# Kernel tuning notes

Hardware: AMD Instinct MI355X
Metric: run time of the kernel (lower is better)

The kernel has to match this reference:

```python
import jax, jax.numpy as jnp
import numpy as np

NUM_HEADS = 4
NUM_GROUPS = 32
EPS = 1e-5

def setup_inputs() -> dict:
    key = jax.random.key(0)
    ks = jax.random.split(key, 3)
    B, C, H, W = 16, 512, 32, 32
    x = jax.random.normal(ks[0], (B, C, H, W), dtype=jnp.float32)
    gn_w = jnp.ones((C,), jnp.float32)
    gn_b = jnp.zeros((C,), jnp.float32)
    qkv_w = jax.random.normal(ks[1], (3 * C, C), dtype=jnp.float32) * (C ** -0.5)
    qkv_b = jnp.zeros((3 * C,), jnp.float32)
    proj_w = jax.random.normal(ks[2], (C, C), dtype=jnp.float32) * (C ** -0.5)
    proj_b = jnp.zeros((C,), jnp.float32)
    return {"x": x, "gn_w": gn_w, "gn_b": gn_b, "qkv_w": qkv_w,
            "qkv_b": qkv_b, "proj_w": proj_w, "proj_b": proj_b}

def group_norm(x, w, b):
    B, C, H, W = x.shape
    xg = x.reshape(B, NUM_GROUPS, C // NUM_GROUPS, H, W)
    mean = xg.mean(axis=(2, 3, 4), keepdims=True)
    var = xg.var(axis=(2, 3, 4), keepdims=True)
    xg = (xg - mean) * jax.lax.rsqrt(var + EPS)
    x = xg.reshape(B, C, H, W)
    return x * w[None, :, None, None] + b[None, :, None, None]

def reference(x, gn_w, gn_b, qkv_w, qkv_b, proj_w, proj_b):
    B, C, H, W = x.shape
    hd = C // NUM_HEADS
    h = group_norm(x, gn_w, gn_b)
    # 1x1 conv == channel matmul
    qkv = jnp.einsum('oc,bchw->bohw', qkv_w, h) + qkv_b[None, :, None, None]
    q, k, v = jnp.split(qkv, 3, axis=1)
    N = H * W
    q = q.reshape(B, NUM_HEADS, hd, N)
    k = k.reshape(B, NUM_HEADS, hd, N)
    v = v.reshape(B, NUM_HEADS, hd, N)
    scale = hd ** -0.5
    attn = jnp.einsum('bhcn,bhcm->bhnm', q, k) * scale
    attn = jax.nn.softmax(attn, axis=-1)
    o = jnp.einsum('bhnm,bhcm->bhcn', attn, v).reshape(B, C, H, W)
    o = jnp.einsum('oc,bchw->bohw', proj_w, o) + proj_b[None, :, None, None]
    return x + o
```

## Files before the change

### kernel.cpp

```cpp
#include <hip/hip_runtime.h>

typedef __attribute__((ext_vector_type(4))) float f32x4;
typedef __attribute__((ext_vector_type(8))) short s16x8;

#define MFMA16(a, b, c) __builtin_amdgcn_mfma_f32_16x16x32_bf16((a), (b), (c), 0, 0, 0)

__device__ __forceinline__ unsigned short f2bf(float f) {
    union { float f; unsigned u; } v; v.f = f;
    unsigned u = v.u + 0x7FFFu + ((v.u >> 16) & 1u);
    return (unsigned short)(u >> 16);
}

__device__ __forceinline__ unsigned cvtpk(float lo, float hi) {
    unsigned r;
    asm("v_cvt_pk_bf16_f32 %0, %1, %2" : "=v"(r) : "v"(lo), "v"(hi));
    return r;
}

__device__ __forceinline__ float exp2f_fast(float x) {
    float r;
    asm("v_exp_f32 %0, %1" : "=v"(r) : "v"(x));
    return r;
}

__device__ __forceinline__ void gll16(const unsigned short* g, unsigned short* l) {
    __builtin_amdgcn_global_load_lds((const __attribute__((address_space(1))) void*)g,
                                     (__attribute__((address_space(3))) void*)l, 16, 0, 0);
}

__global__ __launch_bounds__(256) void k_wconv(const float* __restrict__ qkv_w,
                                               const float* __restrict__ proj_w,
                                               unsigned short* __restrict__ wout) {
    int i = blockIdx.x * 256 + threadIdx.x;
    const int NQ = 3 * 512 * 512;
    float v = (i < NQ) ? qkv_w[i] : proj_w[i - NQ];
    wout[i] = f2bf(v);
}

__global__ __launch_bounds__(256) void k_gnstats(const float* __restrict__ x,
                                                 float* __restrict__ stats) {
    int bg = blockIdx.x;
    const float4* p = (const float4*)(x + (size_t)bg * 16384);
    float s = 0.f, ss = 0.f;
    for (int i = threadIdx.x; i < 4096; i += 256) {
        float4 v = p[i];
        s += v.x + v.y + v.z + v.w;
        ss += v.x * v.x + v.y * v.y + v.z * v.z + v.w * v.w;
    }
    for (int w = 1; w < 64; w <<= 1) { s += __shfl_xor(s, w); ss += __shfl_xor(ss, w); }
    __shared__ float rs[4], rss[4];
    int wid = threadIdx.x >> 6;
    if ((threadIdx.x & 63) == 0) { rs[wid] = s; rss[wid] = ss; }
    __syncthreads();
    if (threadIdx.x == 0) {
        float S = rs[0] + rs[1] + rs[2] + rs[3];
        float SS = rss[0] + rss[1] + rss[2] + rss[3];
        float mean = S * (1.f / 16384.f);
        float var = SS * (1.f / 16384.f) - mean * mean;
        stats[bg * 2] = mean;
        stats[bg * 2 + 1] = rsqrtf(var + 1e-5f);
    }
}

__global__ __launch_bounds__(256) void k_gnapply(const float* __restrict__ x,
                                                 const float* __restrict__ gnw,
                                                 const float* __restrict__ gnb,
                                                 const float* __restrict__ stats,
                                                 unsigned short* __restrict__ h_t) {
    int b = blockIdx.x >> 5, nb = blockIdx.x & 31;
    int n0 = nb * 32;
    __shared__ unsigned short lds[32][520];
    int t = threadIdx.x;
    int f4 = t & 7, c0 = t >> 3;
    for (int c = c0; c < 512; c += 32) {
        int g = c >> 4;
        float mean = stats[(b * 32 + g) * 2], rstd = stats[(b * 32 + g) * 2 + 1];
        float sc = gnw[c] * rstd;
        float sh = gnb[c] - mean * sc;
        float4 v = *(const float4*)(x + ((size_t)(b * 512 + c)) * 1024 + n0 + f4 * 4);
        lds[f4 * 4 + 0][c] = f2bf(v.x * sc + sh);
        lds[f4 * 4 + 1][c] = f2bf(v.y * sc + sh);
        lds[f4 * 4 + 2][c] = f2bf(v.z * sc + sh);
        lds[f4 * 4 + 3][c] = f2bf(v.w * sc + sh);
    }
    __syncthreads();
    int ch = t & 63;
    for (int nl = t >> 6; nl < 32; nl += 4) {
        *(uint4*)(h_t + ((size_t)(b * 1024 + n0 + nl)) * 512 + ch * 8) =
            *(const uint4*)(&lds[nl][ch * 8]);
    }
}

__global__ __launch_bounds__(256) void k_gemm(const unsigned short* __restrict__ A,
                                              const unsigned short* __restrict__ Bt,
                                              const float* __restrict__ bias, int mode,
                                              unsigned short* __restrict__ Qo,
                                              unsigned short* __restrict__ Ko,
                                              unsigned short* __restrict__ Vo,
                                              const float* __restrict__ xres,
                                              float* __restrict__ out) {
    const int Kd = 512;
    int mt = blockIdx.x, nt = blockIdx.y;
    int t = threadIdx.x, wid = t >> 6, lane = t & 63;
    int lm = lane & 15, q4 = lane >> 4;
    int wm = wid >> 1, wn = wid & 1;
    __shared__ unsigned short ldsA[2][4096];
    __shared__ unsigned short ldsB[2][4096];
    int m0 = mt * 128, n0 = nt * 128;

    auto stage = [&](int buf, int ks) {
        int k0 = ks * 32;
#pragma unroll
        for (int h = 0; h < 2; ++h) {
            int cib = h * 256 + wid * 64;
            int ci = cib + lane;
            int r = ci >> 2;
            int cc = (ci & 3) ^ (r & 3);
            gll16(A + (size_t)(m0 + r) * Kd + k0 + cc * 8, &ldsA[buf][cib * 8]);
            gll16(Bt + (size_t)(n0 + r) * Kd + k0 + cc * 8, &ldsB[buf][cib * 8]);
        }
    };

    f32x4 z = {0.f, 0.f, 0.f, 0.f};
    f32x4 acc[4][4];
#pragma unroll
    for (int fi = 0; fi < 4; ++fi)
#pragma unroll
        for (int fj = 0; fj < 4; ++fj) acc[fi][fj] = z;

    stage(0, 0);
    __syncthreads();
    const int NK = 16;
    for (int ks = 0; ks < NK; ++ks) {
        int cur = ks & 1;
        if (ks + 1 < NK) stage(cur ^ 1, ks + 1);
        const unsigned short* lA = ldsA[cur];
        const unsigned short* lB = ldsB[cur];
        s16x8 af[4], bg[4];
#pragma unroll
        for (int fi = 0; fi < 4; ++fi) {
            int rA = wm * 64 + fi * 16 + lm;
            af[fi] = *(const s16x8*)&lA[(rA * 4 + (q4 ^ (lm & 3))) * 8];
        }
#pragma unroll
        for (int fj = 0; fj < 4; ++fj) {
            int rB = wn * 64 + fj * 16 + lm;
            bg[fj] = *(const s16x8*)&lB[(rB * 4 + (q4 ^ (lm & 3))) * 8];
        }
#pragma unroll
        for (int fi = 0; fi < 4; ++fi)
#pragma unroll
            for (int fj = 0; fj < 4; ++fj) acc[fi][fj] = MFMA16(af[fi], bg[fj], acc[fi][fj]);
        __syncthreads();
    }

    if (mode == 0) {
        int part = mt >> 2;
        int head = mt & 3;
        int b = nt >> 3;
        int bh = b * 4 + head;
        const float qscale = 0.08838834764831845f * 1.4426950408889634f;
#pragma unroll
        for (int fi = 0; fi < 4; ++fi) {
            int ddb = wm * 64 + fi * 16 + 4 * q4;
            float bv[4];
#pragma unroll
            for (int i = 0; i < 4; ++i) bv[i] = bias[mt * 128 + ddb + i];
#pragma unroll
            for (int fj = 0; fj < 4; ++fj) {
                int n = ((nt & 7) << 7) + wn * 64 + fj * 16 + lm;
                f32x4 v = acc[fi][fj];
                if (part == 0) {
                    uint2 pr;
                    pr.x = cvtpk((v[0] + bv[0]) * qscale, (v[1] + bv[1]) * qscale);
                    pr.y = cvtpk((v[2] + bv[2]) * qscale, (v[3] + bv[3]) * qscale);
                    *(uint2*)(Qo + ((size_t)bh * 1024 + n) * 128 + ddb) = pr;
                } else if (part == 1) {
                    uint2 pr;
                    pr.x = cvtpk(v[0] + bv[0], v[1] + bv[1]);
                    pr.y = cvtpk(v[2] + bv[2], v[3] + bv[3]);
                    *(uint2*)(Ko + ((size_t)bh * 1024 + n) * 128 + ddb) = pr;
                } else {
                    int r = (fj & 1) * 16 + lm;
                    int kidx = (lm >> 2) * 8 + (fj & 1) * 4 + (lm & 3);
                    int np = n - r + kidx;
#pragma unroll
                    for (int i = 0; i < 4; ++i)
                        Vo[((size_t)bh * 128 + ddb + i) * 1024 + np] = f2bf(v[i] + bv[i]);
                }
            }
        }
    } else {
        int b = nt >> 3;
#pragma unroll
        for (int fi = 0; fi < 4; ++fi) {
            int ocb = m0 + wm * 64 + fi * 16 + 4 * q4;
            float bv[4];
#pragma unroll
            for (int i = 0; i < 4; ++i) bv[i] = bias[ocb + i];
#pragma unroll
            for (int fj = 0; fj < 4; ++fj) {
                int n = ((nt & 7) << 7) + wn * 64 + fj * 16 + lm;
#pragma unroll
                for (int i = 0; i < 4; ++i) {
                    size_t idx = ((size_t)b * 512 + ocb + i) * 1024 + n;
                    out[idx] = xres[idx] + bv[i] + acc[fi][fj][i];
                }
            }
        }
    }
}

__global__ __launch_bounds__(256, 2) void k_attn(const unsigned short* __restrict__ Q,
                                                 const unsigned short* __restrict__ K,
                                                 const unsigned short* __restrict__ V,
                                                 unsigned short* __restrict__ o_t) {
    int id = blockIdx.y * 8 + blockIdx.x;
    int bh = (id & 7) + ((id >> 6) << 3);
    int qb = (id >> 3) & 7;
    int t = threadIdx.x, wid = t >> 6, lane = t & 63;
    int lm = lane & 15, q4 = lane >> 4;
    __shared__ unsigned short ldsK[2][4096];
    __shared__ unsigned short ldsV[2][4096];
    const unsigned short* Qg = Q + ((size_t)bh * 1024 + qb * 128 + wid * 32) * 128;
    const unsigned short* Kg = K + (size_t)bh * 1024 * 128;
    const unsigned short* Vg = V + (size_t)bh * 128 * 1024;

    s16x8 qf0[4], qf1[4];
#pragma unroll
    for (int dc = 0; dc < 4; ++dc) {
        qf0[dc] = *(const s16x8*)&Qg[lm * 128 + dc * 32 + q4 * 8];
        qf1[dc] = *(const s16x8*)&Qg[(16 + lm) * 128 + dc * 32 + q4 * 8];
    }

    const unsigned short* gk[2];
    const unsigned short* gv[2];
    unsigned short* lkd[2][2];
    unsigned short* lvd[2][2];
#pragma unroll
    for (int h = 0; h < 2; ++h) {
        int cib = h * 256 + wid * 64;
        int ci = cib + lane;
        int mr = ci >> 4, cl = ci & 15;
        gk[h] = Kg + mr * 128 + (cl ^ (mr & 7)) * 8;
        int d = ci >> 2, kc = ci & 3;
        gv[h] = Vg + (size_t)d * 1024 + (kc ^ ((d >> 1) & 3)) * 8;
        lkd[0][h] = &ldsK[0][cib * 8];
        lkd[1][h] = &ldsK[1][cib * 8];
        lvd[0][h] = &ldsV[0][cib * 8];
        lvd[1][h] = &ldsV[1][cib * 8];
    }
    gll16(gk[0], lkd[0][0]); gll16(gk[1], lkd[0][1]);
    gll16(gv[0], lvd[0][0]); gll16(gv[1], lvd[0][1]);
    gk[0] += 4096; gk[1] += 4096; gv[0] += 32; gv[1] += 32;

    f32x4 z = {0.f, 0.f, 0.f, 0.f};
    f32x4 oa[8], ob[8];
#pragma unroll
    for (int i = 0; i < 8; ++i) { oa[i] = z; ob[i] = z; }
    float mra = -1e30f, mrb = -1e30f, lpa = 0.f, lpb = 0.f;

    for (int ms = 0; ms < 32; ++ms) {
        int cur = ms & 1;
        if (ms < 31) {
            int nb = cur ^ 1;
            gll16(gk[0], lkd[nb][0]); gll16(gk[1], lkd[nb][1]);
            gll16(gv[0], lvd[nb][0]); gll16(gv[1], lvd[nb][1]);
            gk[0] += 4096; gk[1] += 4096; gv[0] += 32; gv[1] += 32;
            asm volatile("s_waitcnt vmcnt(4)" ::: "memory");
        } else {
            asm volatile("s_waitcnt vmcnt(0)" ::: "memory");
        }
        __builtin_amdgcn_s_barrier();
        const unsigned short* lK = ldsK[cur];
        const unsigned short* lV = ldsV[cur];

        f32x4 s0a = z, s0b = z, s1a = z, s1b = z;
        __builtin_amdgcn_s_setprio(1);
#pragma unroll
        for (int dc = 0; dc < 4; ++dc) {
            int sw = ((dc * 4 + q4) ^ (lm & 7)) * 8;
            s16x8 k0 = *(const s16x8*)&lK[lm * 128 + sw];
            s16x8 k1 = *(const s16x8*)&lK[(16 + lm) * 128 + sw];
            s0a = MFMA16(k0, qf0[dc], s0a);
            s0b = MFMA16(k0, qf1[dc], s0b);
            s1a = MFMA16(k1, qf0[dc], s1a);
            s1b = MFMA16(k1, qf1[dc], s1b);
        }
        __builtin_amdgcn_s_setprio(0);

        float tma = fmaxf(fmaxf(fmaxf(s0a[0], s0a[1]), fmaxf(s0a[2], s0a[3])),
                          fmaxf(fmaxf(s1a[0], s1a[1]), fmaxf(s1a[2], s1a[3])));
        float tmb = fmaxf(fmaxf(fmaxf(s0b[0], s0b[1]), fmaxf(s0b[2], s0b[3])),
                          fmaxf(fmaxf(s1b[0], s1b[1]), fmaxf(s1b[2], s1b[3])));
        if (!__all(tma <= mra + 8.f && tmb <= mrb + 8.f)) {
            tma = fmaxf(tma, __shfl_xor(tma, 16));
            tma = fmaxf(tma, __shfl_xor(tma, 32));
            tmb = fmaxf(tmb, __shfl_xor(tmb, 16));
            tmb = fmaxf(tmb, __shfl_xor(tmb, 32));
            float mna = fmaxf(mra, tma), mnb = fmaxf(mrb, tmb);
            float ca = exp2f_fast(mra - mna), cb = exp2f_fast(mrb - mnb);
            lpa *= ca; lpb *= cb;
#pragma unroll
            for (int t8 = 0; t8 < 8; ++t8)
#pragma unroll
                for (int i = 0; i < 4; ++i) { oa[t8][i] *= ca; ob[t8][i] *= cb; }
            mra = mna; mrb = mnb;
        }
        float pa[8], pb[8];
#pragma unroll
        for (int i = 0; i < 4; ++i) {
            pa[i]     = exp2f_fast(s0a[i] - mra);
            pa[4 + i] = exp2f_fast(s1a[i] - mra);
            pb[i]     = exp2f_fast(s0b[i] - mrb);
            pb[4 + i] = exp2f_fast(s1b[i] - mrb);
        }
#pragma unroll
        for (int i = 0; i < 8; ++i) { lpa += pa[i]; lpb += pb[i]; }
        union { s16x8 v; unsigned u[4]; } fa, fb;
        fa.u[0] = cvtpk(pa[0], pa[1]); fa.u[1] = cvtpk(pa[2], pa[3]);
        fa.u[2] = cvtpk(pa[4], pa[5]); fa.u[3] = cvtpk(pa[6], pa[7]);
        fb.u[0] = cvtpk(pb[0], pb[1]); fb.u[1] = cvtpk(pb[2], pb[3]);
        fb.u[2] = cvtpk(pb[4], pb[5]); fb.u[3] = cvtpk(pb[6], pb[7]);

        __builtin_amdgcn_s_setprio(1);
#pragma unroll
        for (int t8 = 0; t8 < 8; ++t8) {
            int r = t8 * 16 + lm;
            s16x8 vf = *(const s16x8*)&lV[r * 32 + ((q4 ^ ((lm >> 1) & 3)) * 8)];
            oa[t8] = MFMA16(vf, fa.v, oa[t8]);
            ob[t8] = MFMA16(vf, fb.v, ob[t8]);
        }
        __builtin_amdgcn_s_setprio(0);
        __builtin_amdgcn_s_barrier();
    }

    lpa += __shfl_xor(lpa, 16); lpa += __shfl_xor(lpa, 32);
    lpb += __shfl_xor(lpb, 16); lpb += __shfl_xor(lpb, 32);
    float inva = 1.f / lpa, invb = 1.f / lpb;
    int b = bh >> 2, head = bh & 3;
    size_t rowa = (size_t)b * 1024 + qb * 128 + wid * 32 + lm;
    unsigned short* da = o_t + rowa * 512 + head * 128;
    unsigned short* db = da + (size_t)16 * 512;
#pragma unroll
    for (int t8 = 0; t8 < 8; ++t8) {
        uint2 pr;
        pr.x = cvtpk(oa[t8][0] * inva, oa[t8][1] * inva);
        pr.y = cvtpk(oa[t8][2] * inva, oa[t8][3] * inva);
        *(uint2*)&da[t8 * 16 + q4 * 4] = pr;
        pr.x = cvtpk(ob[t8][0] * invb, ob[t8][1] * invb);
        pr.y = cvtpk(ob[t8][2] * invb, ob[t8][3] * invb);
        *(uint2*)&db[t8 * 16 + q4 * 4] = pr;
    }
}

extern "C" void kernel_launch(void* const* d_in, const int* in_sizes, int n_in,
                              void* d_out, int out_size, void* d_ws, size_t ws_size,
                              hipStream_t stream) {
    const float* x = (const float*)d_in[0];
    const float* gnw = (const float*)d_in[1];
    const float* gnb = (const float*)d_in[2];
    const float* qkvw = (const float*)d_in[3];
    const float* qkvb = (const float*)d_in[4];
    const float* projw = (const float*)d_in[5];
    const float* projb = (const float*)d_in[6];
    float* out = (float*)d_out;
    char* ws = (char*)d_ws;

    unsigned short* wq = (unsigned short*)(ws);
    unsigned short* wp = (unsigned short*)(ws + 1572864);
    float* stats = (float*)(ws + 2097152);
    unsigned short* ht = (unsigned short*)(ws + 2101248);
    unsigned short* Qb = (unsigned short*)(ws + 18878464);
    unsigned short* Kb = (unsigned short*)(ws + 35655680);
    unsigned short* Vb = (unsigned short*)(ws + 52432896);
    unsigned short* ot = ht;

    k_wconv<<<dim3(4096), dim3(256), 0, stream>>>(qkvw, projw, wq);
    k_gnstats<<<dim3(512), dim3(256), 0, stream>>>(x, stats);
    k_gnapply<<<dim3(512), dim3(256), 0, stream>>>(x, gnw, gnb, stats, ht);
    k_gemm<<<dim3(12, 128), dim3(256), 0, stream>>>(wq, ht, qkvb, 0, Qb, Kb, Vb, nullptr, nullptr);
    k_attn<<<dim3(8, 64), dim3(256), 0, stream>>>(Qb, Kb, Vb, ot);
    k_gemm<<<dim3(4, 128), dim3(256), 0, stream>>>(wp, ot, projb, 1, nullptr, nullptr, nullptr, x, out);
}
```

Measured before the change: 148.3 us.

## Remap GEMM blocks per XCD and pipeline loads with explicit vmcnt waits

The GEMM grid becomes 1D. Block ids are remapped so that consecutive blocks on the same XCD share an M tile and walk N tiles, which is meant to improve L2 reuse of the weight and activation tiles. The double-buffer loop now issues the next stage's global-to-LDS loads before waiting only on the previous stage (vmcnt(4)), using raw s_barrier instead of __syncthreads and precomputed pointers. This is meant to overlap memory latency with MFMA work. The manual waitcnt logic is fragile: the counts must match the number of outstanding loads exactly, or the code races.

```diff
diff --git a/kernel.cpp b/kernel.cpp
--- a/kernel.cpp
+++ b/kernel.cpp
@@ -100,7 +100,10 @@
                                               const float* __restrict__ xres,
                                               float* __restrict__ out) {
     const int Kd = 512;
-    int mt = blockIdx.x, nt = blockIdx.y;
+    int id = blockIdx.x;
+    int xcd = id & 7, j = id >> 3;
+    int nt = xcd + 8 * (j & 15);
+    int mt = j >> 4;
     int t = threadIdx.x, wid = t >> 6, lane = t & 63;
     int lm = lane & 15, q4 = lane >> 4;
     int wm = wid >> 1, wn = wid & 1;
@@ -108,18 +111,23 @@
     __shared__ unsigned short ldsB[2][4096];
     int m0 = mt * 128, n0 = nt * 128;
 
-    auto stage = [&](int buf, int ks) {
-        int k0 = ks * 32;
-#pragma unroll
-        for (int h = 0; h < 2; ++h) {
-            int cib = h * 256 + wid * 64;
-            int ci = cib + lane;
-            int r = ci >> 2;
-            int cc = (ci & 3) ^ (r & 3);
-            gll16(A + (size_t)(m0 + r) * Kd + k0 + cc * 8, &ldsA[buf][cib * 8]);
-            gll16(Bt + (size_t)(n0 + r) * Kd + k0 + cc * 8, &ldsB[buf][cib * 8]);
-        }
-    };
+    const unsigned short* gA[2];
+    const unsigned short* gB[2];
+    unsigned short* dA[2][2];
+    unsigned short* dB[2][2];
+#pragma unroll
+    for (int h = 0; h < 2; ++h) {
+        int cib = h * 256 + wid * 64;
+        int ci = cib + lane;
+        int r = ci >> 2;
+        int cc = (ci & 3) ^ (r & 3);
+        gA[h] = A + (size_t)(m0 + r) * Kd + cc * 8;
+        gB[h] = Bt + (size_t)(n0 + r) * Kd + cc * 8;
+        dA[0][h] = &ldsA[0][cib * 8];
+        dA[1][h] = &ldsA[1][cib * 8];
+        dB[0][h] = &ldsB[0][cib * 8];
+        dB[1][h] = &ldsB[1][cib * 8];
+    }
 
     f32x4 z = {0.f, 0.f, 0.f, 0.f};
     f32x4 acc[4][4];
@@ -128,12 +136,24 @@
 #pragma unroll
         for (int fj = 0; fj < 4; ++fj) acc[fi][fj] = z;
 
-    stage(0, 0);
-    __syncthreads();
+    gll16(gA[0], dA[0][0]); gll16(gB[0], dB[0][0]);
+    gll16(gA[1], dA[0][1]); gll16(gB[1], dB[0][1]);
+    gA[0] += 32; gA[1] += 32; gB[0] += 32; gB[1] += 32;
+
     const int NK = 16;
     for (int ks = 0; ks < NK; ++ks) {
         int cur = ks & 1;
-        if (ks + 1 < NK) stage(cur ^ 1, ks + 1);
+        if (ks + 1 < NK) {
+            int nb = cur ^ 1;
+            gll16(gA[0], dA[nb][0]); gll16(gB[0], dB[nb][0]);
+            gll16(gA[1], dA[nb][1]); gll16(gB[1], dB[nb][1]);
+            gA[0] += 32; gA[1] += 32; gB[0] += 32; gB[1] += 32;
+            asm volatile("s_waitcnt vmcnt(4)" ::: "memory");
+        } else {
+            asm volatile("s_waitcnt vmcnt(0)" ::: "memory");
+        }
+        __builtin_amdgcn_s_barrier();
+        asm volatile("" ::: "memory");
         const unsigned short* lA = ldsA[cur];
         const unsigned short* lB = ldsB[cur];
         s16x8 af[4], bg[4];
@@ -151,7 +171,8 @@
         for (int fi = 0; fi < 4; ++fi)
 #pragma unroll
             for (int fj = 0; fj < 4; ++fj) acc[fi][fj] = MFMA16(af[fi], bg[fj], acc[fi][fj]);
-        __syncthreads();
+        asm volatile("" ::: "memory");
+        __builtin_amdgcn_s_barrier();
     }
 
     if (mode == 0) {
@@ -379,7 +400,7 @@
     k_wconv<<<dim3(4096), dim3(256), 0, stream>>>(qkvw, projw, wq);
     k_gnstats<<<dim3(512), dim3(256), 0, stream>>>(x, stats);
     k_gnapply<<<dim3(512), dim3(256), 0, stream>>>(x, gnw, gnb, stats, ht);
-    k_gemm<<<dim3(12, 128), dim3(256), 0, stream>>>(wq, ht, qkvb, 0, Qb, Kb, Vb, nullptr, nullptr);
+    k_gemm<<<dim3(1536), dim3(256), 0, stream>>>(wq, ht, qkvb, 0, Qb, Kb, Vb, nullptr, nullptr);
     k_attn<<<dim3(8, 64), dim3(256), 0, stream>>>(Qb, Kb, Vb, ot);
-    k_gemm<<<dim3(4, 128), dim3(256), 0, stream>>>(wp, ot, projb, 1, nullptr, nullptr, nullptr, x, out);
-}
+    k_gemm<<<dim3(512), dim3(256), 0, stream>>>(wp, ot, projb, 1, nullptr, nullptr, nullptr, x, out);
+}
```

Result: faster. 131.4 us (-11.4%).
